# Kernel optimization log

Hardware: AMD Instinct MI355X
Metric: run time of the kernel (lower is better)

## Reference

```python
import jax, jax.numpy as jnp
import numpy as np


def setup_inputs() -> dict:
    key = jax.random.key(0)
    k1, k2, k3, k4 = jax.random.split(key, 4)
    B, S, D, R = 32, 512, 1024, 256
    batch = jax.random.normal(k1, (B, S, D), dtype=jnp.float32)
    # params initialized uniform(-0.05, 0.05) in the original
    proj_L = jax.random.uniform(k2, (D, R), minval=-0.05, maxval=0.05, dtype=jnp.float32)
    proj_R = jax.random.uniform(k3, (R, D), minval=-0.05, maxval=0.05, dtype=jnp.float32)
    bias = jax.random.uniform(k4, (1,), minval=-0.05, maxval=0.05, dtype=jnp.float32)
    return {"batch": batch, "proj_L": proj_L, "proj_R": proj_R, "bias": bias}


def reference(batch, proj_L, proj_R, bias):
    # logits[b,i,j] = batch[b,i] @ (L @ R) @ batch[b,j] + bias
    # Computed as (batch @ L) @ (batch @ R^T)^T -- two batched GEMMs,
    # avoiding the O(B*S^2*D) expanded intermediate of the original.
    # Dropout is identity in eval mode.
    left = jnp.einsum('bsd,dr->bsr', batch, proj_L)   # [B,S,R]
    right = jnp.einsum('rd,btd->brt', proj_R, batch)  # [B,R,S]
    logits = jnp.einsum('bsr,brt->bst', left, right) + bias[0]
    return logits
```

## Files before the change

### kernel.cpp

```cpp
#include <hip/hip_runtime.h>
#include <hip/hip_bf16.h>
#include <stdint.h>

typedef __attribute__((ext_vector_type(8))) __bf16 bf16x8;
typedef __attribute__((ext_vector_type(4))) float f32x4;

static constexpr int Bb = 32, Ss = 512, Dd = 1024, Rr = 256;

__device__ __forceinline__ void gload_lds16(const void* g, void* l) {
  __builtin_amdgcn_global_load_lds(
      (const __attribute__((address_space(1))) void*)g,
      (__attribute__((address_space(3))) void*)l, 16, 0, 0);
}

__global__ __launch_bounds__(256) void prep_kernel(
    const float* __restrict__ L, const float* __restrict__ R,
    __bf16* __restrict__ Bt) {
  int i = blockIdx.x * 256 + threadIdx.x;
  int n = i >> 10;
  int d = i & (Dd - 1);
  float v = (n < Rr) ? L[d * Rr + n] : R[(size_t)(n - Rr) * Dd + d];
  Bt[i] = (__bf16)v;
}

__global__ __launch_bounds__(512, 2) void proj_gemm(
    const float* __restrict__ batch,
    const __bf16* __restrict__ Bt,
    __bf16* __restrict__ outL,
    __bf16* __restrict__ outR) {
  const int s = ((blockIdx.x & 7) << 5) + (blockIdx.x >> 3);
  const int mt = s >> 2;
  const int nt = s & 3;
  const int m0 = mt * 256, n0 = nt * 128;

  __shared__ __align__(16) char smem[98304];

  const int t = threadIdx.x;
  const int lane = t & 63;
  const int wave = t >> 6;
  const int wr = wave >> 1, wc = wave & 1;

  f32x4 acc[4][4] = {};
  f32x4 areg[8];

  auto issueA = [&](int k0) {
#pragma unroll
    for (int q = 0; q < 4; ++q) {
      int e = q * 512 + t;
      int row = e >> 3, g = e & 7;
      const float* src = batch + (size_t)(m0 + row) * Dd + k0 + g * 8;
      areg[2 * q] = *(const f32x4*)src;
      areg[2 * q + 1] = *(const f32x4*)(src + 4);
    }
  };
  auto writeA = [&](int buf) {
    char* Ab = smem + buf * 32768;
#pragma unroll
    for (int q = 0; q < 4; ++q) {
      int e = q * 512 + t;
      int row = e >> 3, g = e & 7;
      int gs = g ^ (row & 7);
      f32x4 f0 = areg[2 * q], f1 = areg[2 * q + 1];
      bf16x8 v;
      v[0] = (__bf16)f0[0]; v[1] = (__bf16)f0[1];
      v[2] = (__bf16)f0[2]; v[3] = (__bf16)f0[3];
      v[4] = (__bf16)f1[0]; v[5] = (__bf16)f1[1];
      v[6] = (__bf16)f1[2]; v[7] = (__bf16)f1[3];
      *(bf16x8*)(Ab + (row * 8 + gs) * 16) = v;
    }
  };
  auto stageB = [&](int buf, int k0) {
    char* Bbuf = smem + 65536 + buf * 16384;
#pragma unroll
    for (int p = 0; p < 2; ++p) {
      int e = p * 512 + t;
      int row = e >> 3, g = e & 7;
      int gs = g ^ (row & 7);
      gload_lds16(Bt + (size_t)(n0 + row) * Dd + k0 + gs * 8,
                  Bbuf + e * 16);
    }
  };
  auto compute = [&](int buf) {
    const char* Ab = smem + buf * 32768;
    const char* Bbuf = smem + 65536 + buf * 16384;
#pragma unroll
    for (int kk = 0; kk < 2; ++kk) {
      const int g = kk * 4 + (lane >> 4);
      bf16x8 a[4], b[4];
#pragma unroll
      for (int m = 0; m < 4; ++m) {
        int row = wr * 64 + m * 16 + (lane & 15);
        a[m] = *(const bf16x8*)(Ab + (row * 8 + (g ^ (row & 7))) * 16);
      }
#pragma unroll
      for (int n = 0; n < 4; ++n) {
        int row = wc * 64 + n * 16 + (lane & 15);
        b[n] = *(const bf16x8*)(Bbuf + (row * 8 + (g ^ (row & 7))) * 16);
      }
#pragma unroll
      for (int m = 0; m < 4; ++m)
#pragma unroll
        for (int n = 0; n < 4; ++n)
          acc[m][n] = __builtin_amdgcn_mfma_f32_16x16x32_bf16(a[m], b[n],
                                                              acc[m][n], 0, 0, 0);
    }
  };

  issueA(0);
  stageB(0, 0);
  writeA(0);
  asm volatile("s_waitcnt vmcnt(0)" ::: "memory");
  asm volatile("s_waitcnt lgkmcnt(0)" ::: "memory");
  __builtin_amdgcn_s_barrier();

  for (int tt = 0; tt < 16; ++tt) {
    const int buf = tt & 1;
    if (tt < 15) {
      issueA(tt * 64 + 64);
      stageB(buf ^ 1, tt * 64 + 64);
    }
    compute(buf);
    if (tt < 15) {
      writeA(buf ^ 1);
      asm volatile("s_waitcnt vmcnt(0)" ::: "memory");
      asm volatile("s_waitcnt lgkmcnt(0)" ::: "memory");
      __builtin_amdgcn_s_barrier();
    }
  }

  __bf16* out = (n0 < Rr) ? outL : outR;
  const int cb = n0 & (Rr - 1);
  const int col = lane & 15, rgrp = lane >> 4;
#pragma unroll
  for (int m = 0; m < 4; ++m) {
    int r0 = m0 + wr * 64 + m * 16 + rgrp * 4;
#pragma unroll
    for (int n = 0; n < 4; ++n) {
      int c = cb + wc * 64 + n * 16 + col;
#pragma unroll
      for (int i = 0; i < 4; ++i)
        out[(size_t)(r0 + i) * Rr + c] = (__bf16)acc[m][n][i];
    }
  }
}

__global__ __launch_bounds__(256, 4) void score_gemm(
    const __bf16* __restrict__ left,
    const __bf16* __restrict__ right,
    const float* __restrict__ biasp,
    float* __restrict__ out) {
  const int nt = blockIdx.x;
  const int mt = blockIdx.y;
  const int bz = blockIdx.z;
  const __bf16* A = left + (size_t)bz * Ss * Rr;
  const __bf16* B = right + (size_t)bz * Ss * Rr;
  float* O = out + (size_t)bz * Ss * Ss;
  const int m0 = mt * 64, n0 = nt * 128;

  __shared__ __align__(16) char smem[24576];

  const int t = threadIdx.x;
  const int lane = t & 63;
  const int wave = t >> 6;
  const int wr = wave >> 1, wc = wave & 1;

  f32x4 acc[2][4] = {};

  for (int it = 0; it < 4; ++it) {
    const int k0 = it * 64;
    __syncthreads();
#pragma unroll
    for (int q = 0; q < 2; ++q) {
      int e = q * 256 + t;
      int row = e >> 3, g = e & 7;
      int gsrc = g ^ (row & 7);
      gload_lds16(A + (size_t)(m0 + row) * Rr + k0 + gsrc * 8, smem + e * 16);
    }
#pragma unroll
    for (int q = 0; q < 4; ++q) {
      int e = q * 256 + t;
      int row = e >> 3, g = e & 7;
      int gsrc = g ^ (row & 7);
      gload_lds16(B + (size_t)(n0 + row) * Rr + k0 + gsrc * 8,
                  smem + 8192 + e * 16);
    }
    __syncthreads();

#pragma unroll
    for (int kk = 0; kk < 2; ++kk) {
      bf16x8 a[2], b[4];
#pragma unroll
      for (int m = 0; m < 2; ++m) {
        int row = wr * 32 + m * 16 + (lane & 15);
        int g = kk * 4 + (lane >> 4);
        a[m] = *(const bf16x8*)(smem + (row * 8 + (g ^ (row & 7))) * 16);
      }
#pragma unroll
      for (int n = 0; n < 4; ++n) {
        int row = wc * 64 + n * 16 + (lane & 15);
        int g = kk * 4 + (lane >> 4);
        b[n] = *(const bf16x8*)(smem + 8192 +
                                (row * 8 + (g ^ (row & 7))) * 16);
      }
#pragma unroll
      for (int m = 0; m < 2; ++m)
#pragma unroll
        for (int n = 0; n < 4; ++n)
          acc[m][n] = __builtin_amdgcn_mfma_f32_16x16x32_bf16(a[m], b[n],
                                                              acc[m][n], 0, 0, 0);
    }
  }

  const float bias = *biasp;
  const int col = lane & 15, rgrp = lane >> 4;
#pragma unroll
  for (int m = 0; m < 2; ++m) {
    int r0 = m0 + wr * 32 + m * 16 + rgrp * 4;
#pragma unroll
    for (int n = 0; n < 4; ++n) {
      int c = n0 + wc * 64 + n * 16 + col;
#pragma unroll
      for (int i = 0; i < 4; ++i)
        O[(size_t)(r0 + i) * Ss + c] = acc[m][n][i] + bias;
    }
  }
}

extern "C" void kernel_launch(void* const* d_in, const int* in_sizes, int n_in,
                              void* d_out, int out_size, void* d_ws,
                              size_t ws_size, hipStream_t stream) {
  const float* batch = (const float*)d_in[0];
  const float* projL = (const float*)d_in[1];
  const float* projR = (const float*)d_in[2];
  const float* bias = (const float*)d_in[3];
  float* out = (float*)d_out;

  char* ws = (char*)d_ws;
  __bf16* left = (__bf16*)(ws);
  __bf16* right = (__bf16*)(ws + 8388608);
  __bf16* Btc = (__bf16*)(ws + 16777216);

  prep_kernel<<<dim3(2048), dim3(256), 0, stream>>>(projL, projR, Btc);
  proj_gemm<<<dim3(256), dim3(512), 0, stream>>>(batch, Btc, left, right);
  score_gemm<<<dim3(4, 8, 32), dim3(256), 0, stream>>>(left, right, bias, out);
}
```

Measured before the change: 51.73 us.

## Retile projection GEMM to 64x512 tiles so each fp32 batch row is read once

The projection GEMM now gives each block 64 rows and all 512 output columns (L and R combined), with each of the 8 waves owning a 64-column slice. Before, the fp32 batch tile was reloaded and converted by four column-tile blocks; now each batch element is read and converted to bf16 once. The cost is a 144KB LDS footprint that limits occupancy to one block per CU. The full 512x64 weight slice is also staged per k-step, so weight traffic through LDS grows per block.

```diff
diff --git a/kernel.cpp b/kernel.cpp
--- a/kernel.cpp
+++ b/kernel.cpp
@@ -23,78 +23,64 @@
   Bt[i] = (__bf16)v;
 }
 
-__global__ __launch_bounds__(512, 2) void proj_gemm(
+__global__ __launch_bounds__(512, 1) void proj_gemm(
     const float* __restrict__ batch,
     const __bf16* __restrict__ Bt,
     __bf16* __restrict__ outL,
     __bf16* __restrict__ outR) {
   const int s = ((blockIdx.x & 7) << 5) + (blockIdx.x >> 3);
-  const int mt = s >> 2;
-  const int nt = s & 3;
-  const int m0 = mt * 256, n0 = nt * 128;
-
-  __shared__ __align__(16) char smem[98304];
+  const int m0 = s * 64;
+
+  __shared__ __align__(16) char smem[147456];
 
   const int t = threadIdx.x;
   const int lane = t & 63;
   const int wave = t >> 6;
-  const int wr = wave >> 1, wc = wave & 1;
 
   f32x4 acc[4][4] = {};
-  f32x4 areg[8];
+  f32x4 areg0, areg1;
+
+  const int arow = t >> 3, ag = t & 7;
+  const int ags = ag ^ (arow & 7);
 
   auto issueA = [&](int k0) {
-#pragma unroll
-    for (int q = 0; q < 4; ++q) {
-      int e = q * 512 + t;
-      int row = e >> 3, g = e & 7;
-      const float* src = batch + (size_t)(m0 + row) * Dd + k0 + g * 8;
-      areg[2 * q] = *(const f32x4*)src;
-      areg[2 * q + 1] = *(const f32x4*)(src + 4);
-    }
+    const float* src = batch + (size_t)(m0 + arow) * Dd + k0 + ag * 8;
+    areg0 = *(const f32x4*)src;
+    areg1 = *(const f32x4*)(src + 4);
   };
   auto writeA = [&](int buf) {
-    char* Ab = smem + buf * 32768;
-#pragma unroll
-    for (int q = 0; q < 4; ++q) {
-      int e = q * 512 + t;
-      int row = e >> 3, g = e & 7;
-      int gs = g ^ (row & 7);
-      f32x4 f0 = areg[2 * q], f1 = areg[2 * q + 1];
-      bf16x8 v;
-      v[0] = (__bf16)f0[0]; v[1] = (__bf16)f0[1];
-      v[2] = (__bf16)f0[2]; v[3] = (__bf16)f0[3];
-      v[4] = (__bf16)f1[0]; v[5] = (__bf16)f1[1];
-      v[6] = (__bf16)f1[2]; v[7] = (__bf16)f1[3];
-      *(bf16x8*)(Ab + (row * 8 + gs) * 16) = v;
-    }
+    bf16x8 v;
+    v[0] = (__bf16)areg0[0]; v[1] = (__bf16)areg0[1];
+    v[2] = (__bf16)areg0[2]; v[3] = (__bf16)areg0[3];
+    v[4] = (__bf16)areg1[0]; v[5] = (__bf16)areg1[1];
+    v[6] = (__bf16)areg1[2]; v[7] = (__bf16)areg1[3];
+    *(bf16x8*)(smem + buf * 8192 + (arow * 8 + ags) * 16) = v;
   };
   auto stageB = [&](int buf, int k0) {
-    char* Bbuf = smem + 65536 + buf * 16384;
-#pragma unroll
-    for (int p = 0; p < 2; ++p) {
+    char* Bbuf = smem + 16384 + buf * 65536;
+#pragma unroll
+    for (int p = 0; p < 8; ++p) {
       int e = p * 512 + t;
       int row = e >> 3, g = e & 7;
       int gs = g ^ (row & 7);
-      gload_lds16(Bt + (size_t)(n0 + row) * Dd + k0 + gs * 8,
-                  Bbuf + e * 16);
+      gload_lds16(Bt + (size_t)row * Dd + k0 + gs * 8, Bbuf + e * 16);
     }
   };
   auto compute = [&](int buf) {
-    const char* Ab = smem + buf * 32768;
-    const char* Bbuf = smem + 65536 + buf * 16384;
+    const char* Ab = smem + buf * 8192;
+    const char* Bbuf = smem + 16384 + buf * 65536;
 #pragma unroll
     for (int kk = 0; kk < 2; ++kk) {
       const int g = kk * 4 + (lane >> 4);
       bf16x8 a[4], b[4];
 #pragma unroll
       for (int m = 0; m < 4; ++m) {
-        int row = wr * 64 + m * 16 + (lane & 15);
+        int row = m * 16 + (lane & 15);
         a[m] = *(const bf16x8*)(Ab + (row * 8 + (g ^ (row & 7))) * 16);
       }
 #pragma unroll
       for (int n = 0; n < 4; ++n) {
-        int row = wc * 64 + n * 16 + (lane & 15);
+        int row = wave * 64 + n * 16 + (lane & 15);
         b[n] = *(const bf16x8*)(Bbuf + (row * 8 + (g ^ (row & 7))) * 16);
       }
 #pragma unroll
@@ -128,15 +114,15 @@
     }
   }
 
-  __bf16* out = (n0 < Rr) ? outL : outR;
-  const int cb = n0 & (Rr - 1);
+  __bf16* out = (wave < 4) ? outL : outR;
+  const int wcb = (wave & 3) * 64;
   const int col = lane & 15, rgrp = lane >> 4;
 #pragma unroll
   for (int m = 0; m < 4; ++m) {
-    int r0 = m0 + wr * 64 + m * 16 + rgrp * 4;
+    int r0 = m0 + m * 16 + rgrp * 4;
 #pragma unroll
     for (int n = 0; n < 4; ++n) {
-      int c = cb + wc * 64 + n * 16 + col;
+      int c = wcb + n * 16 + col;
 #pragma unroll
       for (int i = 0; i < 4; ++i)
         out[(size_t)(r0 + i) * Rr + c] = (__bf16)acc[m][n][i];
```

Result: faster. 49.68 us (-4.0%).
